# Kernel optimization log

Measured on AMD Instinct MI355X. Metric: run time of the kernel, lower is better.

Reference implementation:

```python
import jax, jax.numpy as jnp
import numpy as np

EMBED_DIM = 1024
NUM_HEADS = 16
HEAD_DIM = EMBED_DIM // NUM_HEADS
B, S = 4, 2048


def setup_inputs() -> dict:
    key = jax.random.key(0)
    ks = jax.random.split(key, 11)
    lim = 1.0 / np.sqrt(EMBED_DIM)
    def lin(k, out_dim, in_dim):
        return jax.random.uniform(k, (out_dim, in_dim), jnp.float32, -lim, lim)
    return {
        "query": jax.random.normal(ks[0], (B, S, EMBED_DIM), jnp.float32),
        "Wq": lin(ks[1], EMBED_DIM, EMBED_DIM), "bq": jnp.zeros((EMBED_DIM,), jnp.float32),
        "Wk": lin(ks[2], EMBED_DIM, EMBED_DIM), "bk": jnp.zeros((EMBED_DIM,), jnp.float32),
        "Wv": lin(ks[3], EMBED_DIM, EMBED_DIM), "bv": jnp.zeros((EMBED_DIM,), jnp.float32),
        "Wo": lin(ks[4], EMBED_DIM, EMBED_DIM), "bo": jnp.zeros((EMBED_DIM,), jnp.float32),
        "Wb": lin(ks[5], NUM_HEADS, EMBED_DIM), "bb": jnp.zeros((NUM_HEADS,), jnp.float32),
    }


def reference(query, Wq, bq, Wk, bk, Wv, bv, Wo, bo, Wb, bb):
    b, s, e = query.shape
    h, d = NUM_HEADS, HEAD_DIM
    scale = 1.0 / np.sqrt(d).astype(np.float32)
    # per-(batch, head) beta gate from mean-pooled query
    pooled = jnp.mean(query, axis=1)                       # [B, E]
    betas = jax.nn.sigmoid(pooled @ Wb.T + bb)             # [B, H]
    betas = betas[:, :, None, None]                        # [B, H, 1, 1]
    Q = (query @ Wq.T + bq).reshape(b, s, h, d).transpose(0, 2, 1, 3)
    K = (query @ Wk.T + bk).reshape(b, s, h, d).transpose(0, 2, 1, 3)
    V = (query @ Wv.T + bv).reshape(b, s, h, d).transpose(0, 2, 1, 3)
    scores = jnp.einsum('bhqd,bhkd->bhqk', Q, K) * scale   # [B, H, S, S]
    attn = jax.nn.softmax(scores * betas, axis=-1)
    out = jnp.einsum('bhqk,bhkd->bhqd', attn, V)           # [B, H, S, D]
    out = out.transpose(0, 2, 1, 3).reshape(b, s, e)
    return out @ Wo.T + bo
```

## Files before the change

kernel.cpp:

```cpp
#include <hip/hip_runtime.h>
#include <hip/hip_bf16.h>


typedef __bf16 bf16x8 __attribute__((ext_vector_type(8)));
typedef float f32x4 __attribute__((ext_vector_type(4)));
typedef unsigned short us4 __attribute__((ext_vector_type(4)));
typedef unsigned int u32x4 __attribute__((ext_vector_type(4)));

#define LOG2E 1.4426950408889634f

static __device__ __forceinline__ void gl_lds16(const __bf16* g, __bf16* l) {
  __builtin_amdgcn_global_load_lds(
      (const __attribute__((address_space(1))) unsigned int*)g,
      (__attribute__((address_space(3))) unsigned int*)l, 16, 0, 0);
}

static __device__ __forceinline__ unsigned int cvtpk(float lo, float hi) {
  unsigned int r;
  asm("v_cvt_pk_bf16_f32 %0, %1, %2" : "=v"(r) : "v"(lo), "v"(hi));
  return r;
}

__global__ __launch_bounds__(256) void cast_f32_bf16(const float* __restrict__ src,
                                                     __bf16* __restrict__ dst) {
  const int i = blockIdx.x * 256 + threadIdx.x;
  const f32x4 v = *(const f32x4*)(src + (size_t)i * 4);
  us4 o;
#pragma unroll
  for (int j = 0; j < 4; j++) o[j] = __builtin_bit_cast(unsigned short, (__bf16)v[j]);
  *(us4*)(dst + (size_t)i * 4) = o;
}

__global__ __launch_bounds__(256) void pooled_mean(const float* __restrict__ q,
                                                   float* __restrict__ pooled) {
  const int b = blockIdx.x >> 5;
  const int sc = (blockIdx.x >> 2) & 7;
  const int ec = blockIdx.x & 3;
  const int e = ec * 256 + threadIdx.x;
  const float* p = q + (size_t)b * 2048 * 1024 + (size_t)sc * 256 * 1024 + e;
  float s = 0.f;
  for (int i = 0; i < 256; i++) s += p[(size_t)i * 1024];
  atomicAdd(&pooled[b * 1024 + e], s * (1.0f / 2048.0f));
}

__global__ __launch_bounds__(256) void betas_k(const float* __restrict__ pooled,
                                               const float* __restrict__ Wb,
                                               const float* __restrict__ bb,
                                               float* __restrict__ betas) {
  const int w = threadIdx.x >> 6, l = threadIdx.x & 63;
  const int idx = blockIdx.x * 4 + w;
  const int b = idx >> 4, h = idx & 15;
  float s = 0.f;
  for (int e = l; e < 1024; e += 64) s += pooled[b * 1024 + e] * Wb[h * 1024 + e];
#pragma unroll
  for (int m = 32; m >= 1; m >>= 1) s += __shfl_xor(s, m);
  if (l == 0) betas[idx] = 1.0f / (1.0f + __expf(-(s + bb[h])));
}

template <int EPI>
__global__ __launch_bounds__(256) void gemm_bt(
    const __bf16* __restrict__ A, const __bf16* __restrict__ Bm,
    const float* __restrict__ b0, const float* __restrict__ b1,
    const float* __restrict__ b2, const float* __restrict__ bet,
    __bf16* __restrict__ o0, __bf16* __restrict__ o1, __bf16* __restrict__ o2,
    float* __restrict__ of, const int M, const int N, const int K) {
  __shared__ __bf16 As[128 * 32];
  __shared__ __bf16 Bs[128 * 32];
  const int t = threadIdx.x;
  const int l = t & 63;
  const int w = t >> 6;
  const int wrow = w >> 1, wcol = w & 1;
  const int lr = l & 15, lq = l >> 4;
  const int blockM = blockIdx.y * 128;
  const int blockN = blockIdx.x * 128;
  const __bf16* Ab = A + (size_t)blockM * K;
  const __bf16* Bb = Bm + (size_t)blockN * K;
  const int srow = t >> 2;
  const int scol = (t & 3) * 8;

  f32x4 acc[4][4] = {};

  for (int kt = 0; kt < K; kt += 32) {
    gl_lds16(Ab + (size_t)srow * K + kt + scol, As + t * 8);
    gl_lds16(Ab + (size_t)(srow + 64) * K + kt + scol, As + 2048 + t * 8);
    gl_lds16(Bb + (size_t)srow * K + kt + scol, Bs + t * 8);
    gl_lds16(Bb + (size_t)(srow + 64) * K + kt + scol, Bs + 2048 + t * 8);
    __syncthreads();
    bf16x8 af[4], bf_[4];
#pragma unroll
    for (int i = 0; i < 4; i++)
      af[i] = *(const bf16x8*)&As[(wrow * 64 + i * 16 + lr) * 32 + lq * 8];
#pragma unroll
    for (int i = 0; i < 4; i++)
      bf_[i] = *(const bf16x8*)&Bs[(wcol * 64 + i * 16 + lr) * 32 + lq * 8];
#pragma unroll
    for (int i = 0; i < 4; i++)
#pragma unroll
      for (int j = 0; j < 4; j++)
        acc[i][j] = __builtin_amdgcn_mfma_f32_16x16x32_bf16(af[i], bf_[j], acc[i][j], 0, 0, 0);
    __syncthreads();
  }

  const int row0 = blockM + wrow * 64 + lq * 4;
  const int col0 = blockN + wcol * 64 + lr;
  if (EPI == 0) {
    const int which = blockN >> 10;
    const int b_ = blockM >> 11;
    const float* bias = (which == 0) ? b0 : ((which == 1) ? b1 : b2);
#pragma unroll
    for (int i = 0; i < 4; i++) {
#pragma unroll
      for (int j = 0; j < 4; j++) {
        const int col = col0 + j * 16;
        const int e = col & 1023;
        const int h = e >> 6, d = e & 63;
        const float bv = bias[e];
        if (which == 0) {
          const float qs = bet[b_ * 16 + h] * (0.125f * LOG2E);
#pragma unroll
          for (int jj = 0; jj < 4; jj++) {
            const int row = row0 + i * 16 + jj;
            o0[((size_t)(b_ * 16 + h) * 2048 + (row & 2047)) * 64 + d] =
                (__bf16)((acc[i][j][jj] + bv) * qs);
          }
        } else if (which == 1) {
#pragma unroll
          for (int jj = 0; jj < 4; jj++) {
            const int row = row0 + i * 16 + jj;
            o1[((size_t)(b_ * 16 + h) * 2048 + (row & 2047)) * 64 + d] =
                (__bf16)(acc[i][j][jj] + bv);
          }
        } else {
          const int s0 = (row0 + i * 16) & 2047;
          us4 pk;
#pragma unroll
          for (int jj = 0; jj < 4; jj++)
            pk[jj] = __builtin_bit_cast(unsigned short, (__bf16)(acc[i][j][jj] + bv));
          *(us4*)&o2[((size_t)(b_ * 16 + h) * 64 + d) * 2048 + s0] = pk;
        }
      }
    }
  } else {
#pragma unroll
    for (int i = 0; i < 4; i++) {
#pragma unroll
      for (int j = 0; j < 4; j++) {
        const int col = col0 + j * 16;
        const float bv = b0[col];
#pragma unroll
        for (int jj = 0; jj < 4; jj++) {
          const int row = row0 + i * 16 + jj;
          of[(size_t)row * N + col] = acc[i][j][jj] + bv;
        }
      }
    }
  }
}

__global__ __launch_bounds__(256) void attn_fwd(const __bf16* __restrict__ Q,
                                                const __bf16* __restrict__ Kb,
                                                const __bf16* __restrict__ Vt,
                                                __bf16* __restrict__ AO) {
  __shared__ float smO[2][64][68];
  __shared__ float smD[4][64];

  const int t = threadIdx.x;
  const int w = t >> 6, l = t & 63;
  const int lr = l & 15, lq = l >> 4;
  const int bh = blockIdx.x >> 5;
  const int qb = blockIdx.x & 31;
  const int b = bh >> 4, h = bh & 15;

  const __bf16* Qp = Q + (size_t)bh * (2048 * 64) + (size_t)qb * (64 * 64);
  const __bf16* Kp = Kb + (size_t)bh * (2048 * 64);
  const __bf16* Vp = Vt + (size_t)bh * (64 * 2048);

  bf16x8 aq[4][2];
#pragma unroll
  for (int qf = 0; qf < 4; qf++)
#pragma unroll
    for (int kc = 0; kc < 2; kc++)
      aq[qf][kc] = *(const bf16x8*)&Qp[(qf * 16 + lr) * 64 + kc * 32 + lq * 8];

  f32x4 o[4][4] = {};
  float dAcc[4] = {0.f, 0.f, 0.f, 0.f};

  for (int tile = w; tile < 64; tile += 4) {
    const int kbase = tile * 32;
    bf16x8 vfr[4];
#pragma unroll
    for (int df = 0; df < 4; df++)
      vfr[df] = *(const bf16x8*)&Vp[(size_t)(df * 16 + lr) * 2048 + kbase + lq * 8];
    bf16x8 kfr[2][2];
#pragma unroll
    for (int kf = 0; kf < 2; kf++)
#pragma unroll
      for (int kc = 0; kc < 2; kc++)
        kfr[kf][kc] = *(const bf16x8*)&Kp[(size_t)(kbase + kf * 16 + lr) * 64 + kc * 32 + lq * 8];

#pragma unroll
    for (int qf = 0; qf < 4; qf++) {
      f32x4 st0 = {}, st1 = {};
      st0 = __builtin_amdgcn_mfma_f32_16x16x32_bf16(kfr[0][0], aq[qf][0], st0, 0, 0, 0);
      st0 = __builtin_amdgcn_mfma_f32_16x16x32_bf16(kfr[0][1], aq[qf][1], st0, 0, 0, 0);
      st1 = __builtin_amdgcn_mfma_f32_16x16x32_bf16(kfr[1][0], aq[qf][0], st1, 0, 0, 0);
      st1 = __builtin_amdgcn_mfma_f32_16x16x32_bf16(kfr[1][1], aq[qf][1], st1, 0, 0, 0);
      float p0[4], p1[4];
#pragma unroll
      for (int jj = 0; jj < 4; jj++) p0[jj] = exp2f(st0[jj]);
#pragma unroll
      for (int jj = 0; jj < 4; jj++) p1[jj] = exp2f(st1[jj]);
      dAcc[qf] += ((p0[0] + p0[1]) + (p0[2] + p0[3])) + ((p1[0] + p1[1]) + (p1[2] + p1[3]));
      unsigned int x0 = cvtpk(p0[0], p0[1]), x1 = cvtpk(p0[2], p0[3]);
      unsigned int y0 = cvtpk(p1[0], p1[1]), y1 = cvtpk(p1[2], p1[3]);
      asm("v_permlane32_swap_b32 %0, %1" : "+v"(x0), "+v"(y0));
      asm("v_permlane16_swap_b32 %0, %1" : "+v"(x0), "+v"(y0));
      asm("v_permlane32_swap_b32 %0, %1" : "+v"(x1), "+v"(y1));
      asm("v_permlane16_swap_b32 %0, %1" : "+v"(x1), "+v"(y1));
      u32x4 pw = {x0, x1, y0, y1};
      const bf16x8 pa = __builtin_bit_cast(bf16x8, pw);
#pragma unroll
      for (int df = 0; df < 4; df++)
        o[qf][df] = __builtin_amdgcn_mfma_f32_16x16x32_bf16(pa, vfr[df], o[qf][df], 0, 0, 0);
    }
  }

#pragma unroll
  for (int qf = 0; qf < 4; qf++) {
    float dv = dAcc[qf];
    dv += __shfl_xor(dv, 16);
    dv += __shfl_xor(dv, 32);
    if (lq == 0) smD[w][qf * 16 + lr] = dv;
  }
  if (w >= 2) {
#pragma unroll
    for (int qf = 0; qf < 4; qf++)
#pragma unroll
      for (int df = 0; df < 4; df++)
#pragma unroll
        for (int jj = 0; jj < 4; jj++)
          smO[w - 2][qf * 16 + lq * 4 + jj][df * 16 + lr] = o[qf][df][jj];
  }
  __syncthreads();
  if (w < 2) {
#pragma unroll
    for (int qf = 0; qf < 4; qf++)
#pragma unroll
      for (int df = 0; df < 4; df++)
#pragma unroll
        for (int jj = 0; jj < 4; jj++)
          smO[w][qf * 16 + lq * 4 + jj][df * 16 + lr] += o[qf][df][jj];
  }
  __syncthreads();

  const int q = t >> 2;
  const int dc = (t & 3) * 16;
  const float denom = smD[0][q] + smD[1][q] + smD[2][q] + smD[3][q];
  const float inv = 1.0f / denom;
  __bf16* op = AO + (size_t)b * (2048 * 1024) + (size_t)(qb * 64 + q) * 1024 + h * 64 + dc;
#pragma unroll
  for (int v4 = 0; v4 < 4; v4++) {
    us4 pk;
#pragma unroll
    for (int c = 0; c < 4; c++)
      pk[c] = __builtin_bit_cast(unsigned short,
                (__bf16)((smO[0][q][dc + v4 * 4 + c] + smO[1][q][dc + v4 * 4 + c]) * inv));
    *(us4*)(op + v4 * 4) = pk;
  }
}

extern "C" void kernel_launch(void* const* d_in, const int* in_sizes, int n_in,
                              void* d_out, int out_size, void* d_ws, size_t ws_size,
                              hipStream_t stream) {
  const float* query = (const float*)d_in[0];
  const float* Wq = (const float*)d_in[1];
  const float* bq = (const float*)d_in[2];
  const float* Wk = (const float*)d_in[3];
  const float* bk = (const float*)d_in[4];
  const float* Wv = (const float*)d_in[5];
  const float* bv = (const float*)d_in[6];
  const float* Wo = (const float*)d_in[7];
  const float* bo = (const float*)d_in[8];
  const float* Wb = (const float*)d_in[9];
  const float* bb = (const float*)d_in[10];
  float* out = (float*)d_out;

  char* ws = (char*)d_ws;
  __bf16* Xbf = (__bf16*)(ws);
  __bf16* Wqkv = (__bf16*)(ws + 16777216);
  __bf16* Wob = (__bf16*)(ws + 23068672);
  __bf16* Qb = (__bf16*)(ws + 25165824);
  __bf16* Kbuf = (__bf16*)(ws + 41943040);
  __bf16* Vt = (__bf16*)(ws + 58720256);
  float* pooled = (float*)(ws + 79691776);
  float* betas = (float*)(ws + 79708160);
  __bf16* AO = Xbf;

  hipMemsetAsync(pooled, 0, 4096 * sizeof(float), stream);
  cast_f32_bf16<<<8192, 256, 0, stream>>>(query, Xbf);
  cast_f32_bf16<<<1024, 256, 0, stream>>>(Wq, Wqkv);
  cast_f32_bf16<<<1024, 256, 0, stream>>>(Wk, Wqkv + 1024 * 1024);
  cast_f32_bf16<<<1024, 256, 0, stream>>>(Wv, Wqkv + 2 * 1024 * 1024);
  cast_f32_bf16<<<1024, 256, 0, stream>>>(Wo, Wob);
  pooled_mean<<<128, 256, 0, stream>>>(query, pooled);
  betas_k<<<16, 256, 0, stream>>>(pooled, Wb, bb, betas);
  gemm_bt<0><<<dim3(24, 64), 256, 0, stream>>>(Xbf, Wqkv, bq, bk, bv, betas,
                                               Qb, Kbuf, Vt, nullptr, 8192, 3072, 1024);
  attn_fwd<<<2048, 256, 0, stream>>>(Qb, Kbuf, Vt, AO);
  gemm_bt<1><<<dim3(8, 64), 256, 0, stream>>>(AO, Wob, bo, nullptr, nullptr, nullptr,
                                              nullptr, nullptr, nullptr, out, 8192, 1024, 1024);
}
```

Baseline: 387.1 us.

## Fuse query cast with mean pooling, merge weight casts, halve attention LDS

Fuses the f32-to-bf16 cast of the query into the mean-pooling kernel so the 32 MB query is read once instead of twice, and merges the four weight cast launches into one. The attention kernel switches exp2f to the raw hardware exp instruction and splits the output reduction into two halves over head-dim, shrinking shared memory to raise occupancy at the cost of extra barriers. The new pooled_cast uses scalar 2-byte stores with only 256 blocks, which may coalesce and parallelize less well than the old vectorized cast.

```diff
diff --git a/kernel.cpp b/kernel.cpp
--- a/kernel.cpp
+++ b/kernel.cpp
@@ -5,6 +5,7 @@
 typedef __bf16 bf16x8 __attribute__((ext_vector_type(8)));
 typedef float f32x4 __attribute__((ext_vector_type(4)));
 typedef unsigned short us4 __attribute__((ext_vector_type(4)));
+typedef unsigned short us8 __attribute__((ext_vector_type(8)));
 typedef unsigned int u32x4 __attribute__((ext_vector_type(4)));
 
 #define LOG2E 1.4426950408889634f
@@ -21,26 +22,55 @@
   return r;
 }
 
-__global__ __launch_bounds__(256) void cast_f32_bf16(const float* __restrict__ src,
-                                                     __bf16* __restrict__ dst) {
-  const int i = blockIdx.x * 256 + threadIdx.x;
+static __device__ __forceinline__ float exp2r(float x) {
+#if __has_builtin(__builtin_amdgcn_exp2f)
+  return __builtin_amdgcn_exp2f(x);
+#else
+  float r;
+  asm("v_exp_f32 %0, %1" : "=v"(r) : "v"(x));
+  return r;
+#endif
+}
+
+__global__ __launch_bounds__(256) void pooled_cast(const float* __restrict__ q,
+                                                   float* __restrict__ pooled,
+                                                   __bf16* __restrict__ Xbf) {
+  const int b = blockIdx.x >> 6;
+  const int sc = (blockIdx.x >> 2) & 15;
+  const int ec = blockIdx.x & 3;
+  const int e = ec * 256 + threadIdx.x;
+  const size_t base = (size_t)b * 2048 * 1024 + (size_t)sc * 128 * 1024 + e;
+  const float* p = q + base;
+  __bf16* xo = Xbf + base;
+  float s = 0.f;
+  for (int i = 0; i < 128; i++) {
+    const float v = p[(size_t)i * 1024];
+    s += v;
+    xo[(size_t)i * 1024] = (__bf16)v;
+  }
+  atomicAdd(&pooled[b * 1024 + e], s * (1.0f / 2048.0f));
+}
+
+__global__ __launch_bounds__(256) void cast_w(const float* __restrict__ Wq,
+                                              const float* __restrict__ Wk,
+                                              const float* __restrict__ Wv,
+                                              const float* __restrict__ Wo,
+                                              __bf16* __restrict__ Wqkv,
+                                              __bf16* __restrict__ Wob) {
+  const int which = blockIdx.x >> 10;
+  const int off = blockIdx.x & 1023;
+  const float* src;
+  __bf16* dst;
+  if (which == 0) { src = Wq; dst = Wqkv; }
+  else if (which == 1) { src = Wk; dst = Wqkv + 1024 * 1024; }
+  else if (which == 2) { src = Wv; dst = Wqkv + 2 * 1024 * 1024; }
+  else { src = Wo; dst = Wob; }
+  const int i = off * 256 + threadIdx.x;
   const f32x4 v = *(const f32x4*)(src + (size_t)i * 4);
   us4 o;
 #pragma unroll
   for (int j = 0; j < 4; j++) o[j] = __builtin_bit_cast(unsigned short, (__bf16)v[j]);
   *(us4*)(dst + (size_t)i * 4) = o;
-}
-
-__global__ __launch_bounds__(256) void pooled_mean(const float* __restrict__ q,
-                                                   float* __restrict__ pooled) {
-  const int b = blockIdx.x >> 5;
-  const int sc = (blockIdx.x >> 2) & 7;
-  const int ec = blockIdx.x & 3;
-  const int e = ec * 256 + threadIdx.x;
-  const float* p = q + (size_t)b * 2048 * 1024 + (size_t)sc * 256 * 1024 + e;
-  float s = 0.f;
-  for (int i = 0; i < 256; i++) s += p[(size_t)i * 1024];
-  atomicAdd(&pooled[b * 1024 + e], s * (1.0f / 2048.0f));
 }
 
 __global__ __launch_bounds__(256) void betas_k(const float* __restrict__ pooled,
@@ -161,7 +191,7 @@
                                                 const __bf16* __restrict__ Kb,
                                                 const __bf16* __restrict__ Vt,
                                                 __bf16* __restrict__ AO) {
-  __shared__ float smO[2][64][68];
+  __shared__ float smO[2][64][36];
   __shared__ float smD[4][64];
 
   const int t = threadIdx.x;
@@ -207,9 +237,9 @@
       st1 = __builtin_amdgcn_mfma_f32_16x16x32_bf16(kfr[1][1], aq[qf][1], st1, 0, 0, 0);
       float p0[4], p1[4];
 #pragma unroll
-      for (int jj = 0; jj < 4; jj++) p0[jj] = exp2f(st0[jj]);
-#pragma unroll
-      for (int jj = 0; jj < 4; jj++) p1[jj] = exp2f(st1[jj]);
+      for (int jj = 0; jj < 4; jj++) p0[jj] = exp2r(st0[jj]);
+#pragma unroll
+      for (int jj = 0; jj < 4; jj++) p1[jj] = exp2r(st1[jj]);
       dAcc[qf] += ((p0[0] + p0[1]) + (p0[2] + p0[3])) + ((p1[0] + p1[1]) + (p1[2] + p1[3]));
       unsigned int x0 = cvtpk(p0[0], p0[1]), x1 = cvtpk(p0[2], p0[3]);
       unsigned int y0 = cvtpk(p1[0], p1[1]), y1 = cvtpk(p1[2], p1[3]);
@@ -232,11 +262,17 @@
     dv += __shfl_xor(dv, 32);
     if (lq == 0) smD[w][qf * 16 + lr] = dv;
   }
+
+  const int q = t >> 2;
+  const int c8 = (t & 3) * 8;
+  __bf16* op = AO + (size_t)b * (2048 * 1024) + (size_t)(qb * 64 + q) * 1024 + h * 64;
+  float inv;
+
   if (w >= 2) {
 #pragma unroll
     for (int qf = 0; qf < 4; qf++)
 #pragma unroll
-      for (int df = 0; df < 4; df++)
+      for (int df = 0; df < 2; df++)
 #pragma unroll
         for (int jj = 0; jj < 4; jj++)
           smO[w - 2][qf * 16 + lq * 4 + jj][df * 16 + lr] = o[qf][df][jj];
@@ -246,26 +282,60 @@
 #pragma unroll
     for (int qf = 0; qf < 4; qf++)
 #pragma unroll
-      for (int df = 0; df < 4; df++)
+      for (int df = 0; df < 2; df++)
 #pragma unroll
         for (int jj = 0; jj < 4; jj++)
           smO[w][qf * 16 + lq * 4 + jj][df * 16 + lr] += o[qf][df][jj];
   }
-  __syncthreads();
-
-  const int q = t >> 2;
-  const int dc = (t & 3) * 16;
-  const float denom = smD[0][q] + smD[1][q] + smD[2][q] + smD[3][q];
-  const float inv = 1.0f / denom;
-  __bf16* op = AO + (size_t)b * (2048 * 1024) + (size_t)(qb * 64 + q) * 1024 + h * 64 + dc;
-#pragma unroll
-  for (int v4 = 0; v4 < 4; v4++) {
-    us4 pk;
-#pragma unroll
-    for (int c = 0; c < 4; c++)
-      pk[c] = __builtin_bit_cast(unsigned short,
-                (__bf16)((smO[0][q][dc + v4 * 4 + c] + smO[1][q][dc + v4 * 4 + c]) * inv));
-    *(us4*)(op + v4 * 4) = pk;
+  inv = 1.0f / (smD[0][q] + smD[1][q] + smD[2][q] + smD[3][q]);
+  __syncthreads();
+  {
+    const f32x4 a0 = *(const f32x4*)&smO[0][q][c8];
+    const f32x4 a1 = *(const f32x4*)&smO[0][q][c8 + 4];
+    const f32x4 b0v = *(const f32x4*)&smO[1][q][c8];
+    const f32x4 b1v = *(const f32x4*)&smO[1][q][c8 + 4];
+    us8 pk;
+#pragma unroll
+    for (int c = 0; c < 4; c++) {
+      pk[c] = __builtin_bit_cast(unsigned short, (__bf16)((a0[c] + b0v[c]) * inv));
+      pk[c + 4] = __builtin_bit_cast(unsigned short, (__bf16)((a1[c] + b1v[c]) * inv));
+    }
+    *(us8*)(op + c8) = pk;
+  }
+  __syncthreads();
+
+  if (w >= 2) {
+#pragma unroll
+    for (int qf = 0; qf < 4; qf++)
+#pragma unroll
+      for (int df = 2; df < 4; df++)
+#pragma unroll
+        for (int jj = 0; jj < 4; jj++)
+          smO[w - 2][qf * 16 + lq * 4 + jj][(df - 2) * 16 + lr] = o[qf][df][jj];
+  }
+  __syncthreads();
+  if (w < 2) {
+#pragma unroll
+    for (int qf = 0; qf < 4; qf++)
+#pragma unroll
+      for (int df = 2; df < 4; df++)
+#pragma unroll
+        for (int jj = 0; jj < 4; jj++)
+          smO[w][qf * 16 + lq * 4 + jj][(df - 2) * 16 + lr] += o[qf][df][jj];
+  }
+  __syncthreads();
+  {
+    const f32x4 a0 = *(const f32x4*)&smO[0][q][c8];
+    const f32x4 a1 = *(const f32x4*)&smO[0][q][c8 + 4];
+    const f32x4 b0v = *(const f32x4*)&smO[1][q][c8];
+    const f32x4 b1v = *(const f32x4*)&smO[1][q][c8 + 4];
+    us8 pk;
+#pragma unroll
+    for (int c = 0; c < 4; c++) {
+      pk[c] = __builtin_bit_cast(unsigned short, (__bf16)((a0[c] + b0v[c]) * inv));
+      pk[c + 4] = __builtin_bit_cast(unsigned short, (__bf16)((a1[c] + b1v[c]) * inv));
+    }
+    *(us8*)(op + 32 + c8) = pk;
   }
 }
 
@@ -297,12 +367,8 @@
   __bf16* AO = Xbf;
 
   hipMemsetAsync(pooled, 0, 4096 * sizeof(float), stream);
-  cast_f32_bf16<<<8192, 256, 0, stream>>>(query, Xbf);
-  cast_f32_bf16<<<1024, 256, 0, stream>>>(Wq, Wqkv);
-  cast_f32_bf16<<<1024, 256, 0, stream>>>(Wk, Wqkv + 1024 * 1024);
-  cast_f32_bf16<<<1024, 256, 0, stream>>>(Wv, Wqkv + 2 * 1024 * 1024);
-  cast_f32_bf16<<<1024, 256, 0, stream>>>(Wo, Wob);
-  pooled_mean<<<128, 256, 0, stream>>>(query, pooled);
+  pooled_cast<<<256, 256, 0, stream>>>(query, pooled, Xbf);
+  cast_w<<<4096, 256, 0, stream>>>(Wq, Wk, Wv, Wo, Wqkv, Wob);
   betas_k<<<16, 256, 0, stream>>>(pooled, Wb, bb, betas);
   gemm_bt<0><<<dim3(24, 64), 256, 0, stream>>>(Xbf, Wqkv, bq, bk, bv, betas,
                                                Qb, Kbuf, Vt, nullptr, 8192, 3072, 1024);
```

After: 361.8 us. 1.07x faster.
